# Kernel tuning notes

Measured on AMD Instinct MI355X. Metric: run time of the kernel, lower is better.

The kernel has to match this reference:

```python
import jax, jax.numpy as jnp
import numpy as np

EPS = 1e-5

def _bn(x, gamma, beta):
    # BatchNorm1d training-mode math: batch mean / biased variance over edge dim
    mean = jnp.mean(x, axis=0)
    var = jnp.mean(jnp.square(x - mean), axis=0)
    return (x - mean) * (gamma / jnp.sqrt(var + EPS)) + beta


def setup_inputs() -> dict:
    key = jax.random.key(0)
    ks = jax.random.split(key, 12)
    n, d, s, h, e = 50000, 256, 32, 128, 500000
    feat = 3 * d + s + 1  # 801
    sc = lambda fan_in: 1.0 / np.sqrt(fan_in)
    return {
        "node_embeddings": jax.random.normal(ks[0], (n, d), jnp.float32),
        "gradient_scores": jax.random.normal(ks[1], (e,), jnp.float32),
        "step_embedding": jax.random.normal(ks[2], (s,), jnp.float32),
        "W1": jax.random.normal(ks[3], (feat, h), jnp.float32) * sc(feat),
        "b1": jnp.zeros((h,), jnp.float32),
        "g1": jnp.ones((h,), jnp.float32),
        "be1": jnp.zeros((h,), jnp.float32),
        "W2": jax.random.normal(ks[4], (h, h // 2), jnp.float32) * sc(h),
        "b2": jnp.zeros((h // 2,), jnp.float32),
        "g2": jnp.ones((h // 2,), jnp.float32),
        "be2": jnp.zeros((h // 2,), jnp.float32),
        "W3": jax.random.normal(ks[5], (h // 2, 1), jnp.float32) * sc(h // 2),
        "b3": jnp.zeros((1,), jnp.float32),
        "edge_index": jax.random.randint(ks[6], (2, e), 0, n, jnp.int64),
    }


def reference(node_embeddings, gradient_scores, step_embedding,
              W1, b1, g1, be1, W2, b2, g2, be2, W3, b3, edge_index):
    src, dst = edge_index[0], edge_index[1]
    h_u = node_embeddings[src]              # [E, d]
    h_v = node_embeddings[dst]              # [E, d]
    edge_diff = jnp.abs(h_u - h_v)          # [E, d]
    E = edge_index.shape[1]
    step = jnp.broadcast_to(step_embedding[None, :], (E, step_embedding.shape[0]))
    feats = jnp.concatenate([h_u, h_v, edge_diff, step, gradient_scores[:, None]], axis=1)
    x = jnp.maximum(feats @ W1 + b1, 0.0)
    x = _bn(x, g1, be1)                     # dropout is identity in eval
    x = jnp.maximum(x @ W2 + b2, 0.0)
    x = _bn(x, g2, be2)
    out = jnp.tanh(x @ W3 + b3)[:, 0]       # [E]
    return out
```

## Files before the change

### kernel.cpp

```cpp
#include <hip/hip_runtime.h>

#define NE 500000
#define DIMK 256
#define H1 128
#define H2 64
#define EPSBN 1e-5f
#define GRID1 512
#define NT1 1954
#define NJOBS2 NT1

typedef _Float16 half8 __attribute__((ext_vector_type(8)));
typedef float f32x4 __attribute__((ext_vector_type(4)));
typedef unsigned short ushort8 __attribute__((ext_vector_type(8)));

static __device__ __forceinline__ half8 habs8(half8 x) {
  ushort8 u = __builtin_bit_cast(ushort8, x);
  u &= (unsigned short)0x7FFF;
  return __builtin_bit_cast(half8, u);
}
static __device__ __forceinline__ float h2f(unsigned int u) {
  return (float)__builtin_bit_cast(_Float16, (unsigned short)(u & 0xffff));
}

__global__ void k_prep(const float* __restrict__ W1, const float* __restrict__ b1,
                       const float* __restrict__ step, float* __restrict__ c0) {
  const int j = threadIdx.x;
  if (j < H1) {
    float a = b1[j];
#pragma unroll
    for (int tt = 0; tt < 32; ++tt) a += step[tt] * W1[(768 + tt) * H1 + j];
    c0[j] = a;
  }
}

__global__ void k_prep16(const float* __restrict__ emb, _Float16* __restrict__ embh) {
  const int i = (blockIdx.x * 256 + threadIdx.x) * 8;
  const float4 a = *(const float4*)(emb + i);
  const float4 b = *(const float4*)(emb + i + 4);
  half8 h;
  h[0] = (_Float16)a.x; h[1] = (_Float16)a.y; h[2] = (_Float16)a.z; h[3] = (_Float16)a.w;
  h[4] = (_Float16)b.x; h[5] = (_Float16)b.y; h[6] = (_Float16)b.z; h[7] = (_Float16)b.w;
  *(half8*)(embh + i) = h;
}

__global__ void k_prepB(const float* __restrict__ W1, _Float16* __restrict__ bfrag) {
  const int g = blockIdx.x * 256 + threadIdx.x;
  const int lane = g & 63, f = g >> 6;
  const int c = f & 7, kc = (f >> 3) & 7, s = f >> 6;
  const int row0 = s * 256 + kc * 32 + (lane >> 4) * 8;
  const int col = c * 16 + (lane & 15);
  half8 h;
#pragma unroll
  for (int j = 0; j < 8; ++j) h[j] = (_Float16)W1[(row0 + j) * H1 + col];
  *(half8*)(bfrag + (size_t)g * 8) = h;
}

__global__ __launch_bounds__(256, 2)
void k_layer1(const _Float16* __restrict__ embh, const void* __restrict__ eidx_raw,
              const float* __restrict__ grad, const float* __restrict__ W1,
              const float* __restrict__ c0, const _Float16* __restrict__ bfrag,
              _Float16* __restrict__ x1, float* __restrict__ p1) {
  __shared__ int s_src[256], s_dst[256];
  __shared__ float s_g[256];
  __shared__ float s_wg[128], s_c0[128], s_sum[128], s_sq[128];

  const int t = threadIdx.x, bid = blockIdx.x;
  const int w = t >> 6, lane = t & 63, quad = lane >> 4, m15 = lane & 15;

  if (t < 128) {
    s_wg[t] = W1[800 * H1 + t];
    s_c0[t] = c0[t];
    s_sum[t] = 0.f; s_sq[t] = 0.f;
  }

  const unsigned* ew = (const unsigned*)eidx_raw;
  const bool is64 = ((ew[1] | ew[3] | ew[5] | ew[7]) == 0u);
  const int* e32 = (const int*)eidx_raw;
  const long long* e64 = (const long long*)eidx_raw;

  float st_s[8] = {0, 0, 0, 0, 0, 0, 0, 0}, st_q[8] = {0, 0, 0, 0, 0, 0, 0, 0};
  const half8* bp = (const half8*)bfrag;

  for (int tile = bid; tile < NT1; tile += GRID1) {
    const int base = tile * 256;
    __syncthreads();
    {
      int e = base + t; if (e >= NE) e = NE - 1;
      if (is64) { s_src[t] = (int)e64[e]; s_dst[t] = (int)e64[NE + e]; }
      else      { s_src[t] = e32[e];      s_dst[t] = e32[NE + e]; }
      s_g[t] = grad[e];
    }
    __syncthreads();

    const int r0 = w * 64 + m15;
    const _Float16* pu[4];
    const _Float16* pv[4];
#pragma unroll
    for (int r = 0; r < 4; ++r) {
      pu[r] = embh + (size_t)s_src[r0 + r * 16] * DIMK + quad * 8;
      pv[r] = embh + (size_t)s_dst[r0 + r * 16] * DIMK + quad * 8;
    }
    f32x4 acc[4][8];
#pragma unroll
    for (int r = 0; r < 4; ++r)
#pragma unroll
      for (int c = 0; c < 8; ++c) acc[r][c] = (f32x4)0.f;

#pragma unroll 1
    for (int kc = 0; kc < 8; ++kc) {
      half8 u[4], v[4], d[4];
#pragma unroll
      for (int r = 0; r < 4; ++r) {
        u[r] = *(const half8*)(pu[r] + kc * 32);
        v[r] = *(const half8*)(pv[r] + kc * 32);
      }
#pragma unroll
      for (int r = 0; r < 4; ++r) d[r] = habs8(u[r] - v[r]);

      half8 bu = bp[(kc * 8 + 0) * 64 + lane];
      half8 bv = bp[(64 + kc * 8 + 0) * 64 + lane];
      half8 bd = bp[(128 + kc * 8 + 0) * 64 + lane];
#pragma unroll
      for (int c = 0; c < 8; ++c) {
        half8 nbu, nbv, nbd;
        if (c < 7) {
          nbu = bp[(kc * 8 + c + 1) * 64 + lane];
          nbv = bp[(64 + kc * 8 + c + 1) * 64 + lane];
          nbd = bp[(128 + kc * 8 + c + 1) * 64 + lane];
        }
#pragma unroll
        for (int r = 0; r < 4; ++r)
          acc[r][c] = __builtin_amdgcn_mfma_f32_16x16x32_f16(u[r], bu, acc[r][c], 0, 0, 0);
#pragma unroll
        for (int r = 0; r < 4; ++r)
          acc[r][c] = __builtin_amdgcn_mfma_f32_16x16x32_f16(v[r], bv, acc[r][c], 0, 0, 0);
#pragma unroll
        for (int r = 0; r < 4; ++r)
          acc[r][c] = __builtin_amdgcn_mfma_f32_16x16x32_f16(d[r], bd, acc[r][c], 0, 0, 0);
        if (c < 7) { bu = nbu; bv = nbv; bd = nbd; }
      }
    }
#pragma unroll
    for (int r = 0; r < 4; ++r) {
      const int erow = w * 64 + r * 16 + quad * 4;
#pragma unroll
      for (int c = 0; c < 8; ++c) {
        const int colL = c * 16 + m15;
        const float wgv = s_wg[colL], c0v = s_c0[colL];
#pragma unroll
        for (int reg = 0; reg < 4; ++reg) {
          const int e = base + erow + reg;
          float x = acc[r][c][reg] + s_g[erow + reg] * wgv + c0v;
          x = fmaxf(x, 0.f);
          if (e >= NE) x = 0.f;
          st_s[c] += x; st_q[c] += x * x;
          if (e < NE) x1[(size_t)e * H1 + colL] = (_Float16)x;
        }
      }
    }
  }
  __syncthreads();
#pragma unroll
  for (int c = 0; c < 8; ++c) {
    float a = st_s[c]; a += __shfl_xor(a, 16); a += __shfl_xor(a, 32);
    float b = st_q[c]; b += __shfl_xor(b, 16); b += __shfl_xor(b, 32);
    if (lane < 16) { atomicAdd(&s_sum[c * 16 + m15], a); atomicAdd(&s_sq[c * 16 + m15], b); }
  }
  __syncthreads();
  if (t < 128) {
    p1[t * GRID1 + bid] = s_sum[t];
    p1[128 * GRID1 + t * GRID1 + bid] = s_sq[t];
  }
}

__global__ void k_fin1(const float* __restrict__ p1, const float* __restrict__ g1,
                       const float* __restrict__ be1, const float* __restrict__ W2,
                       const float* __restrict__ b2, float* __restrict__ w2f,
                       float* __restrict__ b2f) {
  __shared__ float s1[128], t1[128];
  const int t = threadIdx.x;
  if (t < 128) {
    float s = 0.f, q = 0.f;
    const float4* rs = (const float4*)(p1 + t * GRID1);
    const float4* rq = (const float4*)(p1 + 128 * GRID1 + t * GRID1);
#pragma unroll 4
    for (int i = 0; i < GRID1 / 4; ++i) {
      float4 a = rs[i]; s += a.x + a.y + a.z + a.w;
      float4 b = rq[i]; q += b.x + b.y + b.z + b.w;
    }
    const float inv = 1.0f / (float)NE;
    float mean = s * inv;
    float var = q * inv - mean * mean;
    float sc = g1[t] * rsqrtf(var + EPSBN);
    s1[t] = sc; t1[t] = be1[t] - mean * sc;
  }
  __syncthreads();
  for (int i = t; i < H1 * H2; i += 256) w2f[i] = s1[i >> 6] * W2[i];
  if (t < 64) {
    float b = b2[t];
    for (int j = 0; j < 128; ++j) b += t1[j] * W2[j * 64 + t];
    b2f[t] = b;
  }
}

__global__ __launch_bounds__(256, 2)
void k_layer2(const _Float16* __restrict__ x1, const float* __restrict__ w2f,
              const float* __restrict__ b2f, _Float16* __restrict__ x2,
              float* __restrict__ p2) {
  __shared__ __align__(16) _Float16 b_lds[8192];
  __shared__ float s_b[64], s_sum[64], s_sq[64];
  const int t = threadIdx.x, bid = blockIdx.x;
  const int w = t >> 6, lane = t & 63, quad = lane >> 4, m15 = lane & 15;

  for (int i = t; i < 8192; i += 256) {
    const int j = i & 7, li = (i >> 3) & 63, f = i >> 9;
    const int c = f & 3, kk = f >> 2;
    const int row = kk * 32 + (li >> 4) * 8 + j;
    const int col = c * 16 + (li & 15);
    b_lds[i] = (_Float16)w2f[row * H2 + col];
  }
  if (t < 64) { s_b[t] = b2f[t]; s_sum[t] = 0.f; s_sq[t] = 0.f; }
  __syncthreads();

  float st_s[4] = {0, 0, 0, 0}, st_q[4] = {0, 0, 0, 0};
  const half8* bp = (const half8*)b_lds;

  for (int job = bid; job < NJOBS2; job += GRID1) {
    const int base = job * 256;
    const _Float16* pa[4];
#pragma unroll
    for (int r = 0; r < 4; ++r) {
      int e = base + w * 64 + r * 16 + m15; if (e >= NE) e = NE - 1;
      pa[r] = x1 + (size_t)e * H1 + quad * 8;
    }
    f32x4 acc[4][4];
#pragma unroll
    for (int r = 0; r < 4; ++r)
#pragma unroll
      for (int c = 0; c < 4; ++c) acc[r][c] = (f32x4)0.f;

#pragma unroll
    for (int kk = 0; kk < 4; ++kk) {
      half8 a[4];
#pragma unroll
      for (int r = 0; r < 4; ++r) a[r] = *(const half8*)(pa[r] + kk * 32);
#pragma unroll
      for (int c = 0; c < 4; ++c) {
        const half8 bf = bp[(kk * 4 + c) * 64 + lane];
#pragma unroll
        for (int r = 0; r < 4; ++r)
          acc[r][c] = __builtin_amdgcn_mfma_f32_16x16x32_f16(a[r], bf, acc[r][c], 0, 0, 0);
      }
    }
#pragma unroll
    for (int r = 0; r < 4; ++r) {
      const int erow = w * 64 + r * 16 + quad * 4;
#pragma unroll
      for (int c = 0; c < 4; ++c) {
        const int colL = c * 16 + m15;
        const float bv = s_b[colL];
#pragma unroll
        for (int reg = 0; reg < 4; ++reg) {
          const int e = base + erow + reg;
          float x = acc[r][c][reg] + bv;
          x = fmaxf(x, 0.f);
          if (e >= NE) x = 0.f;
          st_s[c] += x; st_q[c] += x * x;
          if (e < NE) x2[(size_t)e * H2 + colL] = (_Float16)x;
        }
      }
    }
  }
  __syncthreads();
#pragma unroll
  for (int c = 0; c < 4; ++c) {
    float a = st_s[c]; a += __shfl_xor(a, 16); a += __shfl_xor(a, 32);
    float b = st_q[c]; b += __shfl_xor(b, 16); b += __shfl_xor(b, 32);
    if (lane < 16) { atomicAdd(&s_sum[c * 16 + m15], a); atomicAdd(&s_sq[c * 16 + m15], b); }
  }
  __syncthreads();
  if (t < 64) {
    p2[t * 512 + bid] = s_sum[t];
    p2[64 * 512 + t * 512 + bid] = s_sq[t];
  }
}

__global__ void k_fin2(const float* __restrict__ p2, const float* __restrict__ g2,
                       const float* __restrict__ be2, const float* __restrict__ W3,
                       const float* __restrict__ b3, float* __restrict__ w3f,
                       float* __restrict__ b3f) {
  __shared__ float tp[64];
  const int t = threadIdx.x;
  if (t < 64) {
    float s = 0.f, q = 0.f;
    const float4* rs = (const float4*)(p2 + t * 512);
    const float4* rq = (const float4*)(p2 + 64 * 512 + t * 512);
#pragma unroll 4
    for (int i = 0; i < 128; ++i) {
      float4 a = rs[i]; s += a.x + a.y + a.z + a.w;
      float4 b = rq[i]; q += b.x + b.y + b.z + b.w;
    }
    const float inv = 1.0f / (float)NE;
    float mean = s * inv;
    float var = q * inv - mean * mean;
    float sc = g2[t] * rsqrtf(var + EPSBN);
    float tt = be2[t] - mean * sc;
    w3f[t] = sc * W3[t];
    tp[t] = tt * W3[t];
  }
  __syncthreads();
  if (t == 0) {
    float b = b3[0];
    for (int j = 0; j < 64; ++j) b += tp[j];
    b3f[0] = b;
  }
}

__global__ __launch_bounds__(256)
void k_out(const unsigned short* __restrict__ x2, const float* __restrict__ w3f,
           const float* __restrict__ b3f, float* __restrict__ out) {
  __shared__ float s_w[64];
  __shared__ float s_b;
  const int t = threadIdx.x;
  if (t < 64) s_w[t] = w3f[t];
  if (t == 0) s_b = b3f[0];
  __syncthreads();
  const int gid = blockIdx.x * 256 + t;
  const int e = gid >> 2, p = gid & 3;
  if (e < NE) {
    const uint4* r = (const uint4*)(x2 + (size_t)e * H2 + p * 16);
    float s = 0.f;
#pragma unroll
    for (int i = 0; i < 2; ++i) {
      const uint4 u = r[i];
      const int jb = p * 16 + i * 8;
      s += h2f(u.x) * s_w[jb + 0] + h2f(u.x >> 16) * s_w[jb + 1];
      s += h2f(u.y) * s_w[jb + 2] + h2f(u.y >> 16) * s_w[jb + 3];
      s += h2f(u.z) * s_w[jb + 4] + h2f(u.z >> 16) * s_w[jb + 5];
      s += h2f(u.w) * s_w[jb + 6] + h2f(u.w >> 16) * s_w[jb + 7];
    }
    s += __shfl_xor(s, 1);
    s += __shfl_xor(s, 2);
    if (p == 0) out[e] = tanhf(s + s_b);
  }
}

extern "C" void kernel_launch(void* const* d_in, const int* in_sizes, int n_in,
                              void* d_out, int out_size, void* d_ws, size_t ws_size,
                              hipStream_t stream) {
  const float* emb  = (const float*)d_in[0];
  const float* grad = (const float*)d_in[1];
  const float* step = (const float*)d_in[2];
  const float* W1   = (const float*)d_in[3];
  const float* b1   = (const float*)d_in[4];
  const float* g1   = (const float*)d_in[5];
  const float* be1  = (const float*)d_in[6];
  const float* W2   = (const float*)d_in[7];
  const float* b2   = (const float*)d_in[8];
  const float* g2   = (const float*)d_in[9];
  const float* be2  = (const float*)d_in[10];
  const float* W3   = (const float*)d_in[11];
  const float* b3   = (const float*)d_in[12];
  const void*  eidx = (const void*)d_in[13];
  float* out = (float*)d_out;

  char* ws = (char*)d_ws;
  _Float16* embh  = (_Float16*)(ws + 0);
  _Float16* x2    = (_Float16*)(ws + 0);
  _Float16* bfrag = (_Float16*)(ws + 25600000LL);
  float*    c0    = (float*)(ws + 25796608LL);
  _Float16* x1    = (_Float16*)(ws + 64000000LL);
  float* p1  = (float*)(ws + 192000000LL);
  float* p2  = (float*)(ws + 192524288LL);
  float* w2f = (float*)(ws + 192786432LL);
  float* b2f = (float*)(ws + 192819200LL);
  float* w3f = (float*)(ws + 192819456LL);
  float* b3f = (float*)(ws + 192819712LL);

  k_prep  <<<1,    256, 0, stream>>>(W1, b1, step, c0);
  k_prep16<<<6250, 256, 0, stream>>>(emb, embh);
  k_prepB <<<48,   256, 0, stream>>>(W1, bfrag);
  k_layer1<<<GRID1,256, 0, stream>>>(embh, eidx, grad, W1, c0, bfrag, x1, p1);
  k_fin1  <<<1,    256, 0, stream>>>(p1, g1, be1, W2, b2, w2f, b2f);
  k_layer2<<<GRID1,256, 0, stream>>>(x1, w2f, b2f, x2, p2);
  k_fin2  <<<1,    128, 0, stream>>>(p2, g2, be2, W3, b3, w3f, b3f);
  k_out   <<<7813, 256, 0, stream>>>((const unsigned short*)x2, w3f, b3f, out);
}
```

Measured before the change: 384.4 us.

## Stage layer-1 weight fragments through double-buffered LDS and re-split layer-2 work

In layer 1, the weight fragments are now staged into a double-buffered LDS area with global_load_lds, prefetching the next k-chunk while the current one is consumed, with barriers between chunks. Before this, every wave re-read its fragments straight from global memory. Layer 2 now uses 128-edge tiles with the four waves split into two row groups and two column groups, 1024 blocks and a launch bound of 4 blocks per CU. That change aims at more occupancy and parallelism, at the cost of each x1 row being loaded by two waves. The extra LDS and the per-chunk barriers in layer 1 could lower occupancy or add sync stalls.

New measurement: 366.4 us. -4.7%, faster.

```diff
diff --git a/kernel.cpp b/kernel.cpp
--- a/kernel.cpp
+++ b/kernel.cpp
@@ -7,11 +7,15 @@
 #define EPSBN 1e-5f
 #define GRID1 512
 #define NT1 1954
-#define NJOBS2 NT1
+#define GRID2 1024
+#define NT2 3907
 
 typedef _Float16 half8 __attribute__((ext_vector_type(8)));
 typedef float f32x4 __attribute__((ext_vector_type(4)));
 typedef unsigned short ushort8 __attribute__((ext_vector_type(8)));
+
+typedef const __attribute__((address_space(1))) void* gas1_t;
+typedef __attribute__((address_space(3))) void* las3_t;
 
 static __device__ __forceinline__ half8 habs8(half8 x) {
   ushort8 u = __builtin_bit_cast(ushort8, x);
@@ -20,6 +24,9 @@
 }
 static __device__ __forceinline__ float h2f(unsigned int u) {
   return (float)__builtin_bit_cast(_Float16, (unsigned short)(u & 0xffff));
+}
+static __device__ __forceinline__ void gload_lds16(const _Float16* src, _Float16* dst) {
+  __builtin_amdgcn_global_load_lds((gas1_t)src, (las3_t)dst, 16, 0, 0);
 }
 
 __global__ void k_prep(const float* __restrict__ W1, const float* __restrict__ b1,
@@ -55,6 +62,16 @@
   *(half8*)(bfrag + (size_t)g * 8) = h;
 }
 
+#define STAGE1(q, kcv) do {                                                   \
+    _Pragma("unroll")                                                         \
+    for (int jj = 0; jj < 6; ++jj) {                                          \
+      const int sc = jj * 4 + w;                                              \
+      const int ff = (sc >> 3) * 64 + (kcv) * 8 + (sc & 7);                   \
+      gload_lds16(bfrag + ((size_t)ff * 64 + lane) * 8,                       \
+                  s_B + (size_t)(q) * 12288 + sc * 512);                      \
+    }                                                                         \
+  } while (0)
+
 __global__ __launch_bounds__(256, 2)
 void k_layer1(const _Float16* __restrict__ embh, const void* __restrict__ eidx_raw,
               const float* __restrict__ grad, const float* __restrict__ W1,
@@ -63,6 +80,7 @@
   __shared__ int s_src[256], s_dst[256];
   __shared__ float s_g[256];
   __shared__ float s_wg[128], s_c0[128], s_sum[128], s_sq[128];
+  __shared__ __align__(16) _Float16 s_B[2 * 12288];
 
   const int t = threadIdx.x, bid = blockIdx.x;
   const int w = t >> 6, lane = t & 63, quad = lane >> 4, m15 = lane & 15;
@@ -79,7 +97,6 @@
   const long long* e64 = (const long long*)eidx_raw;
 
   float st_s[8] = {0, 0, 0, 0, 0, 0, 0, 0}, st_q[8] = {0, 0, 0, 0, 0, 0, 0, 0};
-  const half8* bp = (const half8*)bfrag;
 
   for (int tile = bid; tile < NT1; tile += GRID1) {
     const int base = tile * 256;
@@ -90,6 +107,7 @@
       else      { s_src[t] = e32[e];      s_dst[t] = e32[NE + e]; }
       s_g[t] = grad[e];
     }
+    STAGE1(0, 0);
     __syncthreads();
 
     const int r0 = w * 64 + m15;
@@ -108,6 +126,15 @@
 
 #pragma unroll 1
     for (int kc = 0; kc < 8; ++kc) {
+      if (kc < 7) {
+        STAGE1((kc + 1) & 1, kc + 1);
+        asm volatile("s_waitcnt vmcnt(6)" ::: "memory");
+      } else {
+        asm volatile("s_waitcnt vmcnt(0)" ::: "memory");
+      }
+      __builtin_amdgcn_s_barrier();
+      __builtin_amdgcn_sched_barrier(0);
+
       half8 u[4], v[4], d[4];
 #pragma unroll
       for (int r = 0; r < 4; ++r) {
@@ -117,17 +144,12 @@
 #pragma unroll
       for (int r = 0; r < 4; ++r) d[r] = habs8(u[r] - v[r]);
 
-      half8 bu = bp[(kc * 8 + 0) * 64 + lane];
-      half8 bv = bp[(64 + kc * 8 + 0) * 64 + lane];
-      half8 bd = bp[(128 + kc * 8 + 0) * 64 + lane];
+      const half8* bq = (const half8*)s_B + (size_t)(kc & 1) * 1536 + lane;
 #pragma unroll
       for (int c = 0; c < 8; ++c) {
-        half8 nbu, nbv, nbd;
-        if (c < 7) {
-          nbu = bp[(kc * 8 + c + 1) * 64 + lane];
-          nbv = bp[(64 + kc * 8 + c + 1) * 64 + lane];
-          nbd = bp[(128 + kc * 8 + c + 1) * 64 + lane];
-        }
+        const half8 bu = bq[c * 64];
+        const half8 bv = bq[512 + c * 64];
+        const half8 bd = bq[1024 + c * 64];
 #pragma unroll
         for (int r = 0; r < 4; ++r)
           acc[r][c] = __builtin_amdgcn_mfma_f32_16x16x32_f16(u[r], bu, acc[r][c], 0, 0, 0);
@@ -137,8 +159,9 @@
 #pragma unroll
         for (int r = 0; r < 4; ++r)
           acc[r][c] = __builtin_amdgcn_mfma_f32_16x16x32_f16(d[r], bd, acc[r][c], 0, 0, 0);
-        if (c < 7) { bu = nbu; bv = nbv; bd = nbd; }
-      }
+      }
+      __builtin_amdgcn_sched_barrier(0);
+      __builtin_amdgcn_s_barrier();
     }
 #pragma unroll
     for (int r = 0; r < 4; ++r) {
@@ -203,7 +226,7 @@
   }
 }
 
-__global__ __launch_bounds__(256, 2)
+__global__ __launch_bounds__(256, 4)
 void k_layer2(const _Float16* __restrict__ x1, const float* __restrict__ w2f,
               const float* __restrict__ b2f, _Float16* __restrict__ x2,
               float* __restrict__ p2) {
@@ -211,6 +234,7 @@
   __shared__ float s_b[64], s_sum[64], s_sq[64];
   const int t = threadIdx.x, bid = blockIdx.x;
   const int w = t >> 6, lane = t & 63, quad = lane >> 4, m15 = lane & 15;
+  const int rg = w >> 1, cg = w & 1;
 
   for (int i = t; i < 8192; i += 256) {
     const int j = i & 7, li = (i >> 3) & 63, f = i >> 9;
@@ -222,22 +246,22 @@
   if (t < 64) { s_b[t] = b2f[t]; s_sum[t] = 0.f; s_sq[t] = 0.f; }
   __syncthreads();
 
-  float st_s[4] = {0, 0, 0, 0}, st_q[4] = {0, 0, 0, 0};
+  float st_s[2] = {0, 0}, st_q[2] = {0, 0};
   const half8* bp = (const half8*)b_lds;
 
-  for (int job = bid; job < NJOBS2; job += GRID1) {
-    const int base = job * 256;
+  for (int job = bid; job < NT2; job += GRID2) {
+    const int base = job * 128;
     const _Float16* pa[4];
 #pragma unroll
     for (int r = 0; r < 4; ++r) {
-      int e = base + w * 64 + r * 16 + m15; if (e >= NE) e = NE - 1;
+      int e = base + rg * 64 + r * 16 + m15; if (e >= NE) e = NE - 1;
       pa[r] = x1 + (size_t)e * H1 + quad * 8;
     }
-    f32x4 acc[4][4];
+    f32x4 acc[4][2];
 #pragma unroll
     for (int r = 0; r < 4; ++r)
 #pragma unroll
-      for (int c = 0; c < 4; ++c) acc[r][c] = (f32x4)0.f;
+      for (int c = 0; c < 2; ++c) acc[r][c] = (f32x4)0.f;
 
 #pragma unroll
     for (int kk = 0; kk < 4; ++kk) {
@@ -245,8 +269,8 @@
 #pragma unroll
       for (int r = 0; r < 4; ++r) a[r] = *(const half8*)(pa[r] + kk * 32);
 #pragma unroll
-      for (int c = 0; c < 4; ++c) {
-        const half8 bf = bp[(kk * 4 + c) * 64 + lane];
+      for (int c = 0; c < 2; ++c) {
+        const half8 bf = bp[(kk * 4 + cg * 2 + c) * 64 + lane];
 #pragma unroll
         for (int r = 0; r < 4; ++r)
           acc[r][c] = __builtin_amdgcn_mfma_f32_16x16x32_f16(a[r], bf, acc[r][c], 0, 0, 0);
@@ -254,10 +278,10 @@
     }
 #pragma unroll
     for (int r = 0; r < 4; ++r) {
-      const int erow = w * 64 + r * 16 + quad * 4;
-#pragma unroll
-      for (int c = 0; c < 4; ++c) {
-        const int colL = c * 16 + m15;
+      const int erow = rg * 64 + r * 16 + quad * 4;
+#pragma unroll
+      for (int c = 0; c < 2; ++c) {
+        const int colL = cg * 32 + c * 16 + m15;
         const float bv = s_b[colL];
 #pragma unroll
         for (int reg = 0; reg < 4; ++reg) {
@@ -273,15 +297,18 @@
   }
   __syncthreads();
 #pragma unroll
-  for (int c = 0; c < 4; ++c) {
+  for (int c = 0; c < 2; ++c) {
     float a = st_s[c]; a += __shfl_xor(a, 16); a += __shfl_xor(a, 32);
     float b = st_q[c]; b += __shfl_xor(b, 16); b += __shfl_xor(b, 32);
-    if (lane < 16) { atomicAdd(&s_sum[c * 16 + m15], a); atomicAdd(&s_sq[c * 16 + m15], b); }
+    if (lane < 16) {
+      atomicAdd(&s_sum[cg * 32 + c * 16 + m15], a);
+      atomicAdd(&s_sq[cg * 32 + c * 16 + m15], b);
+    }
   }
   __syncthreads();
   if (t < 64) {
-    p2[t * 512 + bid] = s_sum[t];
-    p2[64 * 512 + t * 512 + bid] = s_sq[t];
+    p2[t * GRID2 + bid] = s_sum[t];
+    p2[64 * GRID2 + t * GRID2 + bid] = s_sq[t];
   }
 }
 
@@ -293,10 +320,10 @@
   const int t = threadIdx.x;
   if (t < 64) {
     float s = 0.f, q = 0.f;
-    const float4* rs = (const float4*)(p2 + t * 512);
-    const float4* rq = (const float4*)(p2 + 64 * 512 + t * 512);
+    const float4* rs = (const float4*)(p2 + t * GRID2);
+    const float4* rq = (const float4*)(p2 + 64 * GRID2 + t * GRID2);
 #pragma unroll 4
-    for (int i = 0; i < 128; ++i) {
+    for (int i = 0; i < GRID2 / 4; ++i) {
       float4 a = rs[i]; s += a.x + a.y + a.z + a.w;
       float4 b = rq[i]; q += b.x + b.y + b.z + b.w;
     }
@@ -369,20 +396,20 @@
   _Float16* x2    = (_Float16*)(ws + 0);
   _Float16* bfrag = (_Float16*)(ws + 25600000LL);
   float*    c0    = (float*)(ws + 25796608LL);
+  float*    p1    = (float*)(ws + 26000000LL);
   _Float16* x1    = (_Float16*)(ws + 64000000LL);
-  float* p1  = (float*)(ws + 192000000LL);
-  float* p2  = (float*)(ws + 192524288LL);
-  float* w2f = (float*)(ws + 192786432LL);
-  float* b2f = (float*)(ws + 192819200LL);
-  float* w3f = (float*)(ws + 192819456LL);
-  float* b3f = (float*)(ws + 192819712LL);
+  float* p2  = (float*)(ws + 192000000LL);
+  float* w2f = (float*)(ws + 192524288LL);
+  float* b2f = (float*)(ws + 192557056LL);
+  float* w3f = (float*)(ws + 192557312LL);
+  float* b3f = (float*)(ws + 192557568LL);
 
   k_prep  <<<1,    256, 0, stream>>>(W1, b1, step, c0);
   k_prep16<<<6250, 256, 0, stream>>>(emb, embh);
   k_prepB <<<48,   256, 0, stream>>>(W1, bfrag);
   k_layer1<<<GRID1,256, 0, stream>>>(embh, eidx, grad, W1, c0, bfrag, x1, p1);
   k_fin1  <<<1,    256, 0, stream>>>(p1, g1, be1, W2, b2, w2f, b2f);
-  k_layer2<<<GRID1,256, 0, stream>>>(x1, w2f, b2f, x2, p2);
+  k_layer2<<<GRID2,256, 0, stream>>>(x1, w2f, b2f, x2, p2);
   k_fin2  <<<1,    128, 0, stream>>>(p2, g2, be2, W3, b3, w3f, b3f);
   k_out   <<<7813, 256, 0, stream>>>((const unsigned short*)x2, w3f, b3f, out);
 }
```

## Software-pipeline layer-1 GEMM with LDS weight staging and gather prefetch

Applied to the files above, without the earlier changes.

Restructures the layer-1 gather-GEMM into an unrolled, double-buffered pipeline. Weight fragments are staged into LDS with global_load_lds, and the next k-chunk's embedding rows are loaded while the current chunk's MFMAs run. The next tile's edge indices and gradient scores are prefetched into registers, which removes the per-tile shared-memory index staging and its barriers. Output stores are packed into 32-bit pairs via lane shuffles. The cost is heavy manual scheduling with explicit vmcnt waits and more LDS, which may lower occupancy and makes correctness depend on the exact wait counts.

New measurement: 494.7 us. 1.29x slower.

```diff
diff --git a/kernel.cpp b/kernel.cpp
--- a/kernel.cpp
+++ b/kernel.cpp
@@ -5,13 +5,18 @@
 #define H1 128
 #define H2 64
 #define EPSBN 1e-5f
+#define TILE1 256
 #define GRID1 512
 #define NT1 1954
-#define NJOBS2 NT1
+#define GRID2 512
+#define NJ2 1954
 
 typedef _Float16 half8 __attribute__((ext_vector_type(8)));
 typedef float f32x4 __attribute__((ext_vector_type(4)));
 typedef unsigned short ushort8 __attribute__((ext_vector_type(8)));
+
+typedef const __attribute__((address_space(1))) void* gas1_t;
+typedef __attribute__((address_space(3))) void* las3_t;
 
 static __device__ __forceinline__ half8 habs8(half8 x) {
   ushort8 u = __builtin_bit_cast(ushort8, x);
@@ -21,6 +26,18 @@
 static __device__ __forceinline__ float h2f(unsigned int u) {
   return (float)__builtin_bit_cast(_Float16, (unsigned short)(u & 0xffff));
 }
+static __device__ __forceinline__ unsigned packf16(float a, float b) {
+  unsigned lo = (unsigned)__builtin_bit_cast(unsigned short, (_Float16)a);
+  unsigned hi = (unsigned)__builtin_bit_cast(unsigned short, (_Float16)b);
+  return lo | (hi << 16);
+}
+static __device__ __forceinline__ void gload_lds16(const _Float16* src, _Float16* dst) {
+  __builtin_amdgcn_global_load_lds((gas1_t)src, (las3_t)dst, 16, 0, 0);
+}
+
+#define WAITV(N) asm volatile("s_waitcnt vmcnt(" #N ")" ::: "memory")
+#define SB0 __builtin_amdgcn_sched_barrier(0)
+#define MF(a, b, c) __builtin_amdgcn_mfma_f32_16x16x32_f16(a, b, c, 0, 0, 0)
 
 __global__ void k_prep(const float* __restrict__ W1, const float* __restrict__ b1,
                        const float* __restrict__ step, float* __restrict__ c0) {
@@ -55,13 +72,69 @@
   *(half8*)(bfrag + (size_t)g * 8) = h;
 }
 
+#define STAGE1(q, kcv) do {                                                   \
+    _Pragma("unroll")                                                         \
+    for (int jj = 0; jj < 6; ++jj) {                                          \
+      const int sc = jj * 4 + w;                                              \
+      const int ff = (sc >> 3) * 64 + (kcv) * 8 + (sc & 7);                   \
+      gload_lds16(bfrag + ((size_t)ff * 64 + lane) * 8,                       \
+                  s_B + (size_t)(q) * 12288 + sc * 512);                      \
+    }                                                                         \
+  } while (0)
+
+#define LOADU(kcn) do {                                                       \
+    u[0] = *(const half8*)(embB + (size_t)(uo[0] + (kcn) * 64));              \
+    u[1] = *(const half8*)(embB + (size_t)(uo[1] + (kcn) * 64));              \
+    u[2] = *(const half8*)(embB + (size_t)(uo[2] + (kcn) * 64));              \
+    u[3] = *(const half8*)(embB + (size_t)(uo[3] + (kcn) * 64));              \
+  } while (0)
+#define LOADV(kcn) do {                                                       \
+    v[0] = *(const half8*)(embB + (size_t)(vo[0] + (kcn) * 64));              \
+    v[1] = *(const half8*)(embB + (size_t)(vo[1] + (kcn) * 64));              \
+    v[2] = *(const half8*)(embB + (size_t)(vo[2] + (kcn) * 64));              \
+    v[3] = *(const half8*)(embB + (size_t)(vo[3] + (kcn) * 64));              \
+  } while (0)
+
+#define KC(kc, NW, ...) do {                                                  \
+    WAITV(NW); SB0;                                                           \
+    __builtin_amdgcn_s_barrier(); SB0;                                        \
+    if ((kc) < 7) { STAGE1(((kc) + 1) & 1, (kc) + 1); }                       \
+    SB0;                                                                      \
+    {                                                                         \
+      half8 d0_ = habs8(u[0] - v[0]), d1_ = habs8(u[1] - v[1]);               \
+      half8 d2_ = habs8(u[2] - v[2]), d3_ = habs8(u[3] - v[3]);               \
+      const half8* bq = (const half8*)s_B + ((kc) & 1) * 1536 + lane;         \
+      _Pragma("unroll")                                                       \
+      for (int c = 0; c < 8; ++c) {                                           \
+        const half8 b_ = bq[c * 64];                                          \
+        acc[0][c] = MF(u[0], b_, acc[0][c]); acc[1][c] = MF(u[1], b_, acc[1][c]); \
+        acc[2][c] = MF(u[2], b_, acc[2][c]); acc[3][c] = MF(u[3], b_, acc[3][c]); \
+      }                                                                       \
+      if ((kc) < 7) { LOADU((kc) + 1); }                                      \
+      _Pragma("unroll")                                                       \
+      for (int c = 0; c < 8; ++c) {                                           \
+        const half8 b_ = bq[512 + c * 64];                                    \
+        acc[0][c] = MF(v[0], b_, acc[0][c]); acc[1][c] = MF(v[1], b_, acc[1][c]); \
+        acc[2][c] = MF(v[2], b_, acc[2][c]); acc[3][c] = MF(v[3], b_, acc[3][c]); \
+      }                                                                       \
+      if ((kc) < 7) { LOADV((kc) + 1); }                                      \
+      _Pragma("unroll")                                                       \
+      for (int c = 0; c < 8; ++c) {                                           \
+        const half8 b_ = bq[1024 + c * 64];                                   \
+        acc[0][c] = MF(d0_, b_, acc[0][c]); acc[1][c] = MF(d1_, b_, acc[1][c]); \
+        acc[2][c] = MF(d2_, b_, acc[2][c]); acc[3][c] = MF(d3_, b_, acc[3][c]); \
+      }                                                                       \
+      __VA_ARGS__                                                             \
+    }                                                                         \
+    SB0;                                                                      \
+  } while (0)
+
 __global__ __launch_bounds__(256, 2)
 void k_layer1(const _Float16* __restrict__ embh, const void* __restrict__ eidx_raw,
               const float* __restrict__ grad, const float* __restrict__ W1,
               const float* __restrict__ c0, const _Float16* __restrict__ bfrag,
               _Float16* __restrict__ x1, float* __restrict__ p1) {
-  __shared__ int s_src[256], s_dst[256];
-  __shared__ float s_g[256];
+  __shared__ __align__(16) _Float16 s_B[2 * 12288];
   __shared__ float s_wg[128], s_c0[128], s_sum[128], s_sq[128];
 
   const int t = threadIdx.x, bid = blockIdx.x;
@@ -77,88 +150,112 @@
   const bool is64 = ((ew[1] | ew[3] | ew[5] | ew[7]) == 0u);
   const int* e32 = (const int*)eidx_raw;
   const long long* e64 = (const long long*)eidx_raw;
+  const char* embB = (const char*)embh;
 
   float st_s[8] = {0, 0, 0, 0, 0, 0, 0, 0}, st_q[8] = {0, 0, 0, 0, 0, 0, 0, 0};
-  const half8* bp = (const half8*)bfrag;
-
-  for (int tile = bid; tile < NT1; tile += GRID1) {
-    const int base = tile * 256;
-    __syncthreads();
-    {
-      int e = base + t; if (e >= NE) e = NE - 1;
-      if (is64) { s_src[t] = (int)e64[e]; s_dst[t] = (int)e64[NE + e]; }
-      else      { s_src[t] = e32[e];      s_dst[t] = e32[NE + e]; }
-      s_g[t] = grad[e];
-    }
-    __syncthreads();
-
-    const int r0 = w * 64 + m15;
-    const _Float16* pu[4];
-    const _Float16* pv[4];
+
+  const int r0 = w * 64 + m15;
+  int tile = bid;
+  int base = tile * TILE1;
+
+  unsigned uo[4], vo[4];
+  {
 #pragma unroll
     for (int r = 0; r < 4; ++r) {
-      pu[r] = embh + (size_t)s_src[r0 + r * 16] * DIMK + quad * 8;
-      pv[r] = embh + (size_t)s_dst[r0 + r * 16] * DIMK + quad * 8;
-    }
+      int ea = base + r0 + r * 16; if (ea >= NE) ea = NE - 1;
+      int cs, cd;
+      if (is64) { cs = (int)e64[ea]; cd = (int)e64[NE + ea]; }
+      else      { cs = e32[ea];      cd = e32[NE + ea]; }
+      uo[r] = (unsigned)cs * 512u + (unsigned)quad * 16u;
+      vo[r] = (unsigned)cd * 512u + (unsigned)quad * 16u;
+    }
+  }
+  SB0;
+  STAGE1(0, 0);
+  SB0;
+  half8 u[4], v[4];
+  LOADU(0); LOADV(0);
+  SB0;
+
+  int ns[4], nd[4];
+  f32x4 gr[4];
+
+  for (; tile < NT1; tile += GRID1) {
+    base = tile * TILE1;
     f32x4 acc[4][8];
 #pragma unroll
     for (int r = 0; r < 4; ++r)
 #pragma unroll
       for (int c = 0; c < 8; ++c) acc[r][c] = (f32x4)0.f;
 
-#pragma unroll 1
-    for (int kc = 0; kc < 8; ++kc) {
-      half8 u[4], v[4], d[4];
-#pragma unroll
+    KC(0, 8, );
+    KC(1, 8, );
+    KC(2, 8, );
+    KC(3, 8, );
+    KC(4, 8, );
+    KC(5, 8, {
+      const int bn = (tile + GRID1 < NT1) ? (tile + GRID1) * TILE1 : 0;
+      _Pragma("unroll")
       for (int r = 0; r < 4; ++r) {
-        u[r] = *(const half8*)(pu[r] + kc * 32);
-        v[r] = *(const half8*)(pv[r] + kc * 32);
-      }
-#pragma unroll
-      for (int r = 0; r < 4; ++r) d[r] = habs8(u[r] - v[r]);
-
-      half8 bu = bp[(kc * 8 + 0) * 64 + lane];
-      half8 bv = bp[(64 + kc * 8 + 0) * 64 + lane];
-      half8 bd = bp[(128 + kc * 8 + 0) * 64 + lane];
-#pragma unroll
-      for (int c = 0; c < 8; ++c) {
-        half8 nbu, nbv, nbd;
-        if (c < 7) {
-          nbu = bp[(kc * 8 + c + 1) * 64 + lane];
-          nbv = bp[(64 + kc * 8 + c + 1) * 64 + lane];
-          nbd = bp[(128 + kc * 8 + c + 1) * 64 + lane];
-        }
-#pragma unroll
-        for (int r = 0; r < 4; ++r)
-          acc[r][c] = __builtin_amdgcn_mfma_f32_16x16x32_f16(u[r], bu, acc[r][c], 0, 0, 0);
-#pragma unroll
-        for (int r = 0; r < 4; ++r)
-          acc[r][c] = __builtin_amdgcn_mfma_f32_16x16x32_f16(v[r], bv, acc[r][c], 0, 0, 0);
-#pragma unroll
-        for (int r = 0; r < 4; ++r)
-          acc[r][c] = __builtin_amdgcn_mfma_f32_16x16x32_f16(d[r], bd, acc[r][c], 0, 0, 0);
-        if (c < 7) { bu = nbu; bv = nbv; bd = nbd; }
-      }
-    }
+        int ea = bn + r0 + r * 16; if (ea >= NE) ea = NE - 1;
+        if (is64) { ns[r] = (int)e64[ea]; nd[r] = (int)e64[NE + ea]; }
+        else      { ns[r] = e32[ea];      nd[r] = e32[NE + ea]; }
+      }
+    });
+    KC(6, 16, {
+      _Pragma("unroll")
+      for (int r = 0; r < 4; ++r) {
+        int ge = base + w * 64 + r * 16 + quad * 4;
+        if (ge > NE - 4) ge = 0;
+        gr[r] = *(const f32x4*)(grad + ge);
+      }
+    });
+    KC(7, 12, );
+
 #pragma unroll
     for (int r = 0; r < 4; ++r) {
-      const int erow = w * 64 + r * 16 + quad * 4;
+      const int e0 = base + w * 64 + r * 16 + quad * 4;
 #pragma unroll
       for (int c = 0; c < 8; ++c) {
         const int colL = c * 16 + m15;
         const float wgv = s_wg[colL], c0v = s_c0[colL];
+        float xv[4];
 #pragma unroll
         for (int reg = 0; reg < 4; ++reg) {
-          const int e = base + erow + reg;
-          float x = acc[r][c][reg] + s_g[erow + reg] * wgv + c0v;
+          float x = acc[r][c][reg] + gr[r][reg] * wgv + c0v;
           x = fmaxf(x, 0.f);
-          if (e >= NE) x = 0.f;
+          if (e0 + reg >= NE) x = 0.f;
+          xv[reg] = x;
           st_s[c] += x; st_q[c] += x * x;
-          if (e < NE) x1[(size_t)e * H1 + colL] = (_Float16)x;
         }
-      }
-    }
-  }
+        unsigned b01 = packf16(xv[0], xv[1]);
+        unsigned b23 = packf16(xv[2], xv[3]);
+        unsigned q01 = (unsigned)__shfl_xor((int)b01, 1);
+        unsigned q23 = (unsigned)__shfl_xor((int)b23, 1);
+        const int ce = colL & ~1;
+        if (!(m15 & 1)) {
+          if (e0 < NE)     *(unsigned*)(x1 + (size_t)e0 * H1 + ce)       = (b01 & 0xffffu) | (q01 << 16);
+          if (e0 + 1 < NE) *(unsigned*)(x1 + (size_t)(e0 + 1) * H1 + ce) = (b01 >> 16) | (q01 & 0xffff0000u);
+        } else {
+          if (e0 + 2 < NE) *(unsigned*)(x1 + (size_t)(e0 + 2) * H1 + ce) = (q23 & 0xffffu) | (b23 << 16);
+          if (e0 + 3 < NE) *(unsigned*)(x1 + (size_t)(e0 + 3) * H1 + ce) = (q23 >> 16) | (b23 & 0xffff0000u);
+        }
+      }
+    }
+    SB0;
+    if (tile + GRID1 < NT1) {
+      STAGE1(0, 0);
+      SB0;
+#pragma unroll
+      for (int r = 0; r < 4; ++r) {
+        uo[r] = (unsigned)ns[r] * 512u + (unsigned)quad * 16u;
+        vo[r] = (unsigned)nd[r] * 512u + (unsigned)quad * 16u;
+      }
+      LOADU(0); LOADV(0);
+      SB0;
+    }
+  }
+
   __syncthreads();
 #pragma unroll
   for (int c = 0; c < 8; ++c) {
@@ -225,7 +322,7 @@
   float st_s[4] = {0, 0, 0, 0}, st_q[4] = {0, 0, 0, 0};
   const half8* bp = (const half8*)b_lds;
 
-  for (int job = bid; job < NJOBS2; job += GRID1) {
+  for (int job = bid; job < NJ2; job += GRID2) {
     const int base = job * 256;
     const _Float16* pa[4];
 #pragma unroll
@@ -369,20 +466,20 @@
   _Float16* x2    = (_Float16*)(ws + 0);
   _Float16* bfrag = (_Float16*)(ws + 25600000LL);
   float*    c0    = (float*)(ws + 25796608LL);
+  float*    p1    = (float*)(ws + 26000000LL);
   _Float16* x1    = (_Float16*)(ws + 64000000LL);
-  float* p1  = (float*)(ws + 192000000LL);
-  float* p2  = (float*)(ws + 192524288LL);
-  float* w2f = (float*)(ws + 192786432LL);
-  float* b2f = (float*)(ws + 192819200LL);
-  float* w3f = (float*)(ws + 192819456LL);
-  float* b3f = (float*)(ws + 192819712LL);
+  float* p2  = (float*)(ws + 192000000LL);
+  float* w2f = (float*)(ws + 192524288LL);
+  float* b2f = (float*)(ws + 192557056LL);
+  float* w3f = (float*)(ws + 192557312LL);
+  float* b3f = (float*)(ws + 192557568LL);
 
   k_prep  <<<1,    256, 0, stream>>>(W1, b1, step, c0);
   k_prep16<<<6250, 256, 0, stream>>>(emb, embh);
   k_prepB <<<48,   256, 0, stream>>>(W1, bfrag);
   k_layer1<<<GRID1,256, 0, stream>>>(embh, eidx, grad, W1, c0, bfrag, x1, p1);
   k_fin1  <<<1,    256, 0, stream>>>(p1, g1, be1, W2, b2, w2f, b2f);
-  k_layer2<<<GRID1,256, 0, stream>>>(x1, w2f, b2f, x2, p2);
+  k_layer2<<<GRID2,256, 0, stream>>>(x1, w2f, b2f, x2, p2);
   k_fin2  <<<1,    128, 0, stream>>>(p2, g2, be2, W3, b3, w3f, b3f);
   k_out   <<<7813, 256, 0, stream>>>((const unsigned short*)x2, w3f, b3f, out);
 }
```
